# Kernel optimization log

Measured on AMD Instinct MI355X. Metric: run time of the kernel, lower is better.

The kernel has to match this reference:

```python
import jax, jax.numpy as jnp
import numpy as np

N_AGENTS = 32
STATE_DIM = 512
EMBED = 64
BATCH = 32768


def setup_inputs() -> dict:
    key = jax.random.key(0)
    ks = jax.random.split(key, 16)
    g = lambda k, shape, fan_in: jax.random.normal(k, shape, jnp.float32) / np.sqrt(fan_in)
    return {
        "agent_qs": jax.random.normal(ks[0], (BATCH, N_AGENTS), jnp.float32),
        "states": jax.random.normal(ks[1], (BATCH, STATE_DIM), jnp.float32),
        # hyper_w1: Linear(state,E) -> ReLU -> Linear(E, n_agents*E)
        "w1_l1_w": g(ks[2], (EMBED, STATE_DIM), STATE_DIM),
        "w1_l1_b": jnp.zeros((EMBED,), jnp.float32),
        "w1_l2_w": g(ks[3], (N_AGENTS * EMBED, EMBED), EMBED),
        "w1_l2_b": jnp.zeros((N_AGENTS * EMBED,), jnp.float32),
        # hyper_w2: Linear(state,E) -> ReLU -> Linear(E, E)
        "w2_l1_w": g(ks[4], (EMBED, STATE_DIM), STATE_DIM),
        "w2_l1_b": jnp.zeros((EMBED,), jnp.float32),
        "w2_l2_w": g(ks[5], (EMBED, EMBED), EMBED),
        "w2_l2_b": jnp.zeros((EMBED,), jnp.float32),
        # hyper_b1: Linear(state, E)
        "b1_w": g(ks[6], (EMBED, STATE_DIM), STATE_DIM),
        "b1_b": jnp.zeros((EMBED,), jnp.float32),
        # hyper_b2: Linear(state,E) -> ReLU -> Linear(E, 1)
        "b2_l1_w": g(ks[7], (EMBED, STATE_DIM), STATE_DIM),
        "b2_l1_b": jnp.zeros((EMBED,), jnp.float32),
        "b2_l2_w": g(ks[8], (1, EMBED), EMBED),
        "b2_l2_b": jnp.zeros((1,), jnp.float32),
    }


def _linear(x, w, b):
    return x @ w.T + b


def reference(agent_qs, states,
              w1_l1_w, w1_l1_b, w1_l2_w, w1_l2_b,
              w2_l1_w, w2_l1_b, w2_l2_w, w2_l2_b,
              b1_w, b1_b, b2_l1_w, b2_l1_b, b2_l2_w, b2_l2_b):
    B = agent_qs.shape[0]
    # hypernetworks producing per-sample weights
    w1 = jnp.abs(_linear(jax.nn.relu(_linear(states, w1_l1_w, w1_l1_b)), w1_l2_w, w1_l2_b))
    w1 = w1.reshape(B, N_AGENTS, EMBED)                      # [B, A, E]
    b1 = _linear(states, b1_w, b1_b)                         # [B, E]
    hidden = jax.nn.elu(jnp.einsum('ba,bae->be', agent_qs, w1) + b1)  # [B, E]
    w2 = jnp.abs(_linear(jax.nn.relu(_linear(states, w2_l1_w, w2_l1_b)), w2_l2_w, w2_l2_b))  # [B, E]
    b2 = _linear(jax.nn.relu(_linear(states, b2_l1_w, b2_l1_b)), b2_l2_w, b2_l2_b)           # [B, 1]
    q_total = jnp.einsum('be,be->b', hidden, w2) + b2[:, 0]  # [B]
    return q_total
```

## Files before the change

### kernel.cpp

```cpp
#include <hip/hip_runtime.h>

typedef unsigned short u16;
typedef unsigned int u32;
typedef short bf16x8 __attribute__((ext_vector_type(8)));
typedef float f32x4 __attribute__((ext_vector_type(4)));
typedef u16 u16x4 __attribute__((ext_vector_type(4)));

#define NAG 32
#define STATE 512
#define EMBED 64
#define TB 64

#define OFF_W1L1 0
#define OFF_W2L1 32768
#define OFF_B1W  65536
#define OFF_B2L1 98304
#define OFF_W1L2 131072
#define OFF_W2L2 262144
#define WS_TOTAL 266240

#define Y_STR    200
#define SB_OFF   12800
#define SB_STR   72
#define SB_BUF   (64 * 72)
#define W1BS_OFF 22016
#define QST_OFF  24064
#define QST_STR  68
#define PBUF_OFF 12800
#define PBUF_STR 72
#define PBUF_WV  (64 * 72)
#define QACC_OFF  31232
#define QACC2_OFF 31360
#define B2WV_OFF  31616
#define SMEM_U16  31744

__device__ __forceinline__ float bf2f(u16 u) {
    u32 i = ((u32)u) << 16; float f;
    __builtin_memcpy(&f, &i, 4); return f;
}
__device__ __forceinline__ u16 f2bf(float f) {
    u32 i; __builtin_memcpy(&i, &f, 4);
    return (u16)((i + 0x8000u) >> 16);
}
__device__ __forceinline__ bf16x8 ld8(const u16* p) {
    return *reinterpret_cast<const bf16x8*>(p);
}
__device__ __forceinline__ bf16x8 cvt8(f32x4 a, f32x4 b) {
    bf16x8 r;
#pragma unroll
    for (int i = 0; i < 4; ++i) r[i]     = (short)f2bf(a[i]);
#pragma unroll
    for (int i = 0; i < 4; ++i) r[i + 4] = (short)f2bf(b[i]);
    return r;
}

__global__ __launch_bounds__(256) void cvt_weights(
    const float* __restrict__ w1l1w, const float* __restrict__ w2l1w,
    const float* __restrict__ b1w,   const float* __restrict__ b2l1w,
    const float* __restrict__ w1l2w, const float* __restrict__ w2l2w,
    u16* __restrict__ ws)
{
    int idx = blockIdx.x * 256 + threadIdx.x;
    const float* src; int off;
    if      (idx < OFF_W2L1)  { src = w1l1w; off = OFF_W1L1; }
    else if (idx < OFF_B1W)   { src = w2l1w; off = OFF_W2L1; }
    else if (idx < OFF_B2L1)  { src = b1w;   off = OFF_B1W;  }
    else if (idx < OFF_W1L2)  { src = b2l1w; off = OFF_B2L1; }
    else if (idx < OFF_W2L2)  { src = w1l2w; off = OFF_W1L2; }
    else if (idx < WS_TOTAL)  { src = w2l2w; off = OFF_W2L2; }
    else return;
    ws[idx] = f2bf(src[idx - off]);
}

__global__ __launch_bounds__(512, 4) void qmix_kernel(
    const float* __restrict__ qs,    const float* __restrict__ st,
    const u16*  __restrict__ wsb,
    const float* __restrict__ w1l1b, const float* __restrict__ w1l2b,
    const float* __restrict__ w2l1b, const float* __restrict__ w2l2b,
    const float* __restrict__ b1b,   const float* __restrict__ b2l1b,
    const float* __restrict__ b2l2w, const float* __restrict__ b2l2b,
    float* __restrict__ out)
{
    __shared__ u16 smem[SMEM_U16];
    float* qaccF  = (float*)(smem + QACC_OFF);
    float* qacc2F = (float*)(smem + QACC2_OFF);
    float* b2wvF  = (float*)(smem + B2WV_OFF);

    const int t    = threadIdx.x;
    const int wave = t >> 6, lane = t & 63;
    const int m = lane & 15, quad = lane >> 4;
    const int sbase = blockIdx.x * TB;

    if (t < 64) b2wvF[t] = b2l2w[t];
    if (t < 256) {
        const float* qp = qs + (size_t)sbase * NAG + t * 8;
        f32x4 q0 = *reinterpret_cast<const f32x4*>(qp);
        f32x4 q1 = *reinterpret_cast<const f32x4*>(qp + 4);
        const int s = t >> 2, a0 = (t & 3) * 8;
#pragma unroll
        for (int j = 0; j < 4; ++j) smem[QST_OFF + (a0 + j) * QST_STR + s]     = f2bf(q0[j]);
#pragma unroll
        for (int j = 0; j < 4; ++j) smem[QST_OFF + (a0 + 4 + j) * QST_STR + s] = f2bf(q1[j]);
    } else {
        const int i = t & 255;
        f32x4 w0 = *reinterpret_cast<const f32x4*>(w1l2b + i * 8);
        f32x4 w1 = *reinterpret_cast<const f32x4*>(w1l2b + i * 8 + 4);
        *reinterpret_cast<bf16x8*>(&smem[W1BS_OFF + i * 8]) = cvt8(w0, w1);
    }

    const int ss1 = t >> 3, c8 = t & 7;
    const float* stb = st + (size_t)sbase * STATE;
    {
        const float* g1 = stb + (size_t)ss1 * STATE + c8 * 8;
        f32x4 a0 = *reinterpret_cast<const f32x4*>(g1);
        f32x4 a1 = *reinterpret_cast<const f32x4*>(g1 + 4);
        *reinterpret_cast<bf16x8*>(&smem[SB_OFF + ss1 * SB_STR + c8 * 8]) = cvt8(a0, a1);
    }

    const u16* wAw = wsb + (size_t)(wave * 32) * STATE;
    bf16x8 bfr[2][2][2];
#pragma unroll
    for (int ot = 0; ot < 2; ++ot) {
        const u16* wr = wAw + (size_t)(ot * 16 + m) * STATE + quad * 8;
        bfr[0][ot][0] = ld8(wr);
        bfr[0][ot][1] = ld8(wr + 32);
    }
    __syncthreads();

    f32x4 acc[4][2] = {};
#pragma unroll
    for (int ks = 0; ks < 8; ++ks) {
        f32x4 sa0 = {}, sa1 = {};
        if (ks < 7) {
            const float* g1 = stb + (size_t)ss1 * STATE + (ks + 1) * 64 + c8 * 8;
            sa0 = *reinterpret_cast<const f32x4*>(g1);
            sa1 = *reinterpret_cast<const f32x4*>(g1 + 4);
#pragma unroll
            for (int ot = 0; ot < 2; ++ot) {
                const u16* wr = wAw + (size_t)(ot * 16 + m) * STATE + (ks + 1) * 64 + quad * 8;
                bfr[(ks + 1) & 1][ot][0] = ld8(wr);
                bfr[(ks + 1) & 1][ot][1] = ld8(wr + 32);
            }
        }
        const u16* sbc = smem + SB_OFF + (ks & 1) * SB_BUF;
#pragma unroll
        for (int st2 = 0; st2 < 4; ++st2) {
            const int row = st2 * 16 + m;
            bf16x8 af0 = ld8(&sbc[row * SB_STR + quad * 8]);
            bf16x8 af1 = ld8(&sbc[row * SB_STR + (quad + 4) * 8]);
#pragma unroll
            for (int ot = 0; ot < 2; ++ot)
                acc[st2][ot] = __builtin_amdgcn_mfma_f32_16x16x32_bf16(af0, bfr[ks & 1][ot][0], acc[st2][ot], 0, 0, 0);
#pragma unroll
            for (int ot = 0; ot < 2; ++ot)
                acc[st2][ot] = __builtin_amdgcn_mfma_f32_16x16x32_bf16(af1, bfr[ks & 1][ot][1], acc[st2][ot], 0, 0, 0);
        }
        if (ks < 7) {
            u16* dst = smem + SB_OFF + ((ks + 1) & 1) * SB_BUF;
            *reinterpret_cast<bf16x8*>(&dst[ss1 * SB_STR + c8 * 8]) = cvt8(sa0, sa1);
        }
        __syncthreads();
    }

    {
        const int grp = wave >> 1, half = wave & 1;
        if (grp < 3) {
            const float* barr = (grp == 0) ? w1l1b : (grp == 1) ? w2l1b : b1b;
            const bool isrelu = (grp != 2);
            float wb[2];
#pragma unroll
            for (int ot = 0; ot < 2; ++ot) wb[ot] = barr[half * 32 + ot * 16 + m];
#pragma unroll
            for (int st2 = 0; st2 < 4; ++st2)
#pragma unroll
                for (int ot = 0; ot < 2; ++ot)
#pragma unroll
                    for (int r = 0; r < 4; ++r) {
                        float v = acc[st2][ot][r] + wb[ot];
                        if (isrelu) v = fmaxf(v, 0.f);
                        smem[(st2 * 16 + quad * 4 + r) * Y_STR + grp * 64 + half * 32 + ot * 16 + m] = f2bf(v);
                    }
        } else {
            float wb[2], bw[2];
#pragma unroll
            for (int ot = 0; ot < 2; ++ot) wb[ot] = b2l1b[half * 32 + ot * 16 + m];
#pragma unroll
            for (int ot = 0; ot < 2; ++ot) bw[ot] = b2wvF[half * 32 + ot * 16 + m];
#pragma unroll
            for (int st2 = 0; st2 < 4; ++st2)
#pragma unroll
                for (int r = 0; r < 4; ++r) {
                    float pd = 0.f;
#pragma unroll
                    for (int ot = 0; ot < 2; ++ot)
                        pd += fmaxf(acc[st2][ot][r] + wb[ot], 0.f) * bw[ot];
#pragma unroll
                    for (int off = 1; off < 16; off <<= 1) pd += __shfl_xor(pd, off, 64);
                    if (m == 0) qacc2F[half * 64 + st2 * 16 + quad * 4 + r] = pd;
                }
        }
    }
    __syncthreads();

    const int ah = wave & 3, sh = wave >> 2;
    bf16x8 h1f[2][2];
#pragma unroll
    for (int st2 = 0; st2 < 2; ++st2) {
        const int row = sh * 32 + st2 * 16 + m;
        h1f[st2][0] = ld8(&smem[row * Y_STR + quad * 8]);
        h1f[st2][1] = ld8(&smem[row * Y_STR + 32 + quad * 8]);
    }

    const u16* wB = wsb + OFF_W1L2 + (size_t)(ah * 8) * 64 * EMBED;
    f32x4 hacc[2][4] = {};
#pragma unroll
    for (int ag = 0; ag < 8; ++ag) {
        const int a = ah * 8 + ag;
        bf16x8 bb[4][2];
#pragma unroll
        for (int ot = 0; ot < 4; ++ot) {
            const u16* wr = wB + (size_t)(ag * 64 + ot * 16 + m) * EMBED + quad * 8;
            bb[ot][0] = ld8(wr);
            bb[ot][1] = ld8(wr + 32);
        }
        float bias[4];
#pragma unroll
        for (int ot = 0; ot < 4; ++ot) bias[ot] = bf2f(smem[W1BS_OFF + a * EMBED + ot * 16 + m]);
#pragma unroll
        for (int st2 = 0; st2 < 2; ++st2) {
            u16x4 qv = *reinterpret_cast<const u16x4*>(
                &smem[QST_OFF + a * QST_STR + sh * 32 + st2 * 16 + quad * 4]);
#pragma unroll
            for (int ot = 0; ot < 4; ++ot) {
                f32x4 p = {};
                p = __builtin_amdgcn_mfma_f32_16x16x32_bf16(h1f[st2][0], bb[ot][0], p, 0, 0, 0);
                p = __builtin_amdgcn_mfma_f32_16x16x32_bf16(h1f[st2][1], bb[ot][1], p, 0, 0, 0);
#pragma unroll
                for (int r = 0; r < 4; ++r)
                    hacc[st2][ot][r] += bf2f((u16)qv[r]) * fabsf(p[r] + bias[ot]);
            }
        }
    }
    __syncthreads();

#pragma unroll
    for (int st2 = 0; st2 < 2; ++st2)
#pragma unroll
        for (int ot = 0; ot < 4; ++ot)
#pragma unroll
            for (int r = 0; r < 4; ++r)
                smem[PBUF_OFF + ah * PBUF_WV
                     + (sh * 32 + st2 * 16 + quad * 4 + r) * PBUF_STR + ot * 16 + m]
                    = f2bf(hacc[st2][ot][r]);
    __syncthreads();

    {
        const int s  = t >> 3;
        const int eb = (t & 7) * 8;
        float v[8];
#pragma unroll
        for (int j = 0; j < 8; ++j) v[j] = 0.f;
#pragma unroll
        for (int pw = 0; pw < 4; ++pw) {
            u16x4 x0 = *reinterpret_cast<const u16x4*>(
                &smem[PBUF_OFF + pw * PBUF_WV + s * PBUF_STR + eb]);
            u16x4 x1 = *reinterpret_cast<const u16x4*>(
                &smem[PBUF_OFF + pw * PBUF_WV + s * PBUF_STR + eb + 4]);
#pragma unroll
            for (int j = 0; j < 4; ++j) v[j]     += bf2f((u16)x0[j]);
#pragma unroll
            for (int j = 0; j < 4; ++j) v[4 + j] += bf2f((u16)x1[j]);
        }
        bf16x8 bv = ld8(&smem[s * Y_STR + 128 + eb]);
        bf16x8 o;
#pragma unroll
        for (int j = 0; j < 8; ++j) {
            float h = v[j] + bf2f((u16)bv[j]);
            h = (h > 0.f) ? h : (__expf(h) - 1.f);
            o[j] = (short)f2bf(h);
        }
        *reinterpret_cast<bf16x8*>(&smem[s * Y_STR + 128 + eb]) = o;
    }
    __syncthreads();

    if (wave < 4) {
        const int s0 = wave * 16;
        bf16x8 h2f0 = ld8(&smem[(s0 + m) * Y_STR + 64 + quad * 8]);
        bf16x8 h2f1 = ld8(&smem[(s0 + m) * Y_STR + 96 + quad * 8]);

        f32x4 qp = {};
#pragma unroll
        for (int tp = 0; tp < 4; ++tp) {
            const u16* wc = wsb + OFF_W2L2 + (size_t)(tp * 16 + m) * EMBED + quad * 8;
            bf16x8 c0 = ld8(wc);
            bf16x8 c1 = ld8(wc + 32);
            f32x4 p = {};
            p = __builtin_amdgcn_mfma_f32_16x16x32_bf16(h2f0, c0, p, 0, 0, 0);
            p = __builtin_amdgcn_mfma_f32_16x16x32_bf16(h2f1, c1, p, 0, 0, 0);
            const float bias = w2l2b[tp * 16 + m];
#pragma unroll
            for (int r = 0; r < 4; ++r)
                qp[r] += bf2f(smem[(s0 + quad * 4 + r) * Y_STR + 128 + tp * 16 + m]) * fabsf(p[r] + bias);
        }
#pragma unroll
        for (int off = 1; off < 16; off <<= 1) {
#pragma unroll
            for (int r = 0; r < 4; ++r) qp[r] += __shfl_xor(qp[r], off, 64);
        }
        if (m == 0) {
#pragma unroll
            for (int r = 0; r < 4; ++r) qaccF[s0 + quad * 4 + r] = qp[r];
        }
    }
    __syncthreads();

    if (t < TB) out[sbase + t] = qaccF[t] + qacc2F[t] + qacc2F[64 + t] + b2l2b[0];
}

extern "C" void kernel_launch(void* const* d_in, const int* in_sizes, int n_in,
                              void* d_out, int out_size, void* d_ws, size_t ws_size,
                              hipStream_t stream)
{
    const float* qs    = (const float*)d_in[0];
    const float* st    = (const float*)d_in[1];
    const float* w1l1w = (const float*)d_in[2];
    const float* w1l1b = (const float*)d_in[3];
    const float* w1l2w = (const float*)d_in[4];
    const float* w1l2b = (const float*)d_in[5];
    const float* w2l1w = (const float*)d_in[6];
    const float* w2l1b = (const float*)d_in[7];
    const float* w2l2w = (const float*)d_in[8];
    const float* w2l2b = (const float*)d_in[9];
    const float* b1w   = (const float*)d_in[10];
    const float* b1b   = (const float*)d_in[11];
    const float* b2l1w = (const float*)d_in[12];
    const float* b2l1b = (const float*)d_in[13];
    const float* b2l2w = (const float*)d_in[14];
    const float* b2l2b = (const float*)d_in[15];

    u16* wsb = (u16*)d_ws;

    cvt_weights<<<(WS_TOTAL + 255) / 256, 256, 0, stream>>>(
        w1l1w, w2l1w, b1w, b2l1w, w1l2w, w2l2w, wsb);

    int B = in_sizes[0] / NAG;
    int grid = B / TB;
    qmix_kernel<<<grid, 512, 0, stream>>>(
        qs, st, wsb,
        w1l1b, w1l2b, w2l1b, w2l2b, b1b, b2l1b, b2l2w, b2l2b,
        (float*)d_out);
}
```

Measured before the change: 168.5 us.

## Halve per-block sample tile and use 256-thread blocks with wider per-wave outputs

Cuts the samples per block from 64 to 32 and the block size from 512 to 256 threads, so the grid doubles. Each wave now computes all 64 outputs of one hypernetwork first layer instead of half of one, and later stages are remapped to match. The register double-buffering of weight fragments is replaced by loading them at the start of each k-step, and the final barrier of the k-loop is dropped. In exchange, the bf16 weights are re-read from cache twice as often per sample, and weight-load latency is less hidden.

```diff
diff --git a/kernel.cpp b/kernel.cpp
--- a/kernel.cpp
+++ b/kernel.cpp
@@ -9,7 +9,7 @@
 #define NAG 32
 #define STATE 512
 #define EMBED 64
-#define TB 64
+#define TB 32
 
 #define OFF_W1L1 0
 #define OFF_W2L1 32768
@@ -19,20 +19,21 @@
 #define OFF_W2L2 262144
 #define WS_TOTAL 266240
 
+#define Y_OFF    0
 #define Y_STR    200
-#define SB_OFF   12800
+#define SB_OFF   6400
 #define SB_STR   72
-#define SB_BUF   (64 * 72)
-#define W1BS_OFF 22016
-#define QST_OFF  24064
-#define QST_STR  68
-#define PBUF_OFF 12800
+#define SB_BUF   (32 * 72)
+#define W1BS_OFF 11008
+#define QST_OFF  13056
+#define QST_STR  36
+#define PBUF_OFF 6400
 #define PBUF_STR 72
-#define PBUF_WV  (64 * 72)
-#define QACC_OFF  31232
-#define QACC2_OFF 31360
-#define B2WV_OFF  31616
-#define SMEM_U16  31744
+#define PBUF_WV  (32 * 72)
+#define QACC_OFF  15616
+#define QACC2_OFF 15680
+#define B2WV_OFF  15744
+#define SMEM_U16  15872
 
 __device__ __forceinline__ float bf2f(u16 u) {
     u32 i = ((u32)u) << 16; float f;
@@ -72,7 +73,7 @@
     ws[idx] = f2bf(src[idx - off]);
 }
 
-__global__ __launch_bounds__(512, 4) void qmix_kernel(
+__global__ __launch_bounds__(256, 4) void qmix_kernel(
     const float* __restrict__ qs,    const float* __restrict__ st,
     const u16*  __restrict__ wsb,
     const float* __restrict__ w1l1b, const float* __restrict__ w1l2b,
@@ -92,7 +93,7 @@
     const int sbase = blockIdx.x * TB;
 
     if (t < 64) b2wvF[t] = b2l2w[t];
-    if (t < 256) {
+    if (t < 128) {
         const float* qp = qs + (size_t)sbase * NAG + t * 8;
         f32x4 q0 = *reinterpret_cast<const f32x4*>(qp);
         f32x4 q1 = *reinterpret_cast<const f32x4*>(qp + 4);
@@ -101,11 +102,11 @@
         for (int j = 0; j < 4; ++j) smem[QST_OFF + (a0 + j) * QST_STR + s]     = f2bf(q0[j]);
 #pragma unroll
         for (int j = 0; j < 4; ++j) smem[QST_OFF + (a0 + 4 + j) * QST_STR + s] = f2bf(q1[j]);
-    } else {
-        const int i = t & 255;
-        f32x4 w0 = *reinterpret_cast<const f32x4*>(w1l2b + i * 8);
-        f32x4 w1 = *reinterpret_cast<const f32x4*>(w1l2b + i * 8 + 4);
-        *reinterpret_cast<bf16x8*>(&smem[W1BS_OFF + i * 8]) = cvt8(w0, w1);
+    }
+    {
+        f32x4 w0 = *reinterpret_cast<const f32x4*>(w1l2b + t * 8);
+        f32x4 w1 = *reinterpret_cast<const f32x4*>(w1l2b + t * 8 + 4);
+        *reinterpret_cast<bf16x8*>(&smem[W1BS_OFF + t * 8]) = cvt8(w0, w1);
     }
 
     const int ss1 = t >> 3, c8 = t & 7;
@@ -117,105 +118,95 @@
         *reinterpret_cast<bf16x8*>(&smem[SB_OFF + ss1 * SB_STR + c8 * 8]) = cvt8(a0, a1);
     }
 
-    const u16* wAw = wsb + (size_t)(wave * 32) * STATE;
-    bf16x8 bfr[2][2][2];
-#pragma unroll
-    for (int ot = 0; ot < 2; ++ot) {
-        const u16* wr = wAw + (size_t)(ot * 16 + m) * STATE + quad * 8;
-        bfr[0][ot][0] = ld8(wr);
-        bfr[0][ot][1] = ld8(wr + 32);
-    }
-    __syncthreads();
-
-    f32x4 acc[4][2] = {};
+    const u16* wAw = wsb + (size_t)(wave * 64) * STATE;
+    __syncthreads();
+
+    f32x4 acc[2][4] = {};
 #pragma unroll
     for (int ks = 0; ks < 8; ++ks) {
+        bf16x8 bfr[4][2];
+#pragma unroll
+        for (int ot = 0; ot < 4; ++ot) {
+            const u16* wr = wAw + (size_t)(ot * 16 + m) * STATE + ks * 64 + quad * 8;
+            bfr[ot][0] = ld8(wr);
+            bfr[ot][1] = ld8(wr + 32);
+        }
         f32x4 sa0 = {}, sa1 = {};
         if (ks < 7) {
             const float* g1 = stb + (size_t)ss1 * STATE + (ks + 1) * 64 + c8 * 8;
             sa0 = *reinterpret_cast<const f32x4*>(g1);
             sa1 = *reinterpret_cast<const f32x4*>(g1 + 4);
-#pragma unroll
-            for (int ot = 0; ot < 2; ++ot) {
-                const u16* wr = wAw + (size_t)(ot * 16 + m) * STATE + (ks + 1) * 64 + quad * 8;
-                bfr[(ks + 1) & 1][ot][0] = ld8(wr);
-                bfr[(ks + 1) & 1][ot][1] = ld8(wr + 32);
-            }
         }
         const u16* sbc = smem + SB_OFF + (ks & 1) * SB_BUF;
 #pragma unroll
-        for (int st2 = 0; st2 < 4; ++st2) {
+        for (int st2 = 0; st2 < 2; ++st2) {
             const int row = st2 * 16 + m;
             bf16x8 af0 = ld8(&sbc[row * SB_STR + quad * 8]);
             bf16x8 af1 = ld8(&sbc[row * SB_STR + (quad + 4) * 8]);
 #pragma unroll
-            for (int ot = 0; ot < 2; ++ot)
-                acc[st2][ot] = __builtin_amdgcn_mfma_f32_16x16x32_bf16(af0, bfr[ks & 1][ot][0], acc[st2][ot], 0, 0, 0);
-#pragma unroll
-            for (int ot = 0; ot < 2; ++ot)
-                acc[st2][ot] = __builtin_amdgcn_mfma_f32_16x16x32_bf16(af1, bfr[ks & 1][ot][1], acc[st2][ot], 0, 0, 0);
+            for (int ot = 0; ot < 4; ++ot)
+                acc[st2][ot] = __builtin_amdgcn_mfma_f32_16x16x32_bf16(af0, bfr[ot][0], acc[st2][ot], 0, 0, 0);
+#pragma unroll
+            for (int ot = 0; ot < 4; ++ot)
+                acc[st2][ot] = __builtin_amdgcn_mfma_f32_16x16x32_bf16(af1, bfr[ot][1], acc[st2][ot], 0, 0, 0);
         }
         if (ks < 7) {
             u16* dst = smem + SB_OFF + ((ks + 1) & 1) * SB_BUF;
             *reinterpret_cast<bf16x8*>(&dst[ss1 * SB_STR + c8 * 8]) = cvt8(sa0, sa1);
-        }
-        __syncthreads();
-    }
-
-    {
-        const int grp = wave >> 1, half = wave & 1;
-        if (grp < 3) {
-            const float* barr = (grp == 0) ? w1l1b : (grp == 1) ? w2l1b : b1b;
-            const bool isrelu = (grp != 2);
-            float wb[2];
-#pragma unroll
-            for (int ot = 0; ot < 2; ++ot) wb[ot] = barr[half * 32 + ot * 16 + m];
-#pragma unroll
-            for (int st2 = 0; st2 < 4; ++st2)
-#pragma unroll
-                for (int ot = 0; ot < 2; ++ot)
-#pragma unroll
-                    for (int r = 0; r < 4; ++r) {
-                        float v = acc[st2][ot][r] + wb[ot];
-                        if (isrelu) v = fmaxf(v, 0.f);
-                        smem[(st2 * 16 + quad * 4 + r) * Y_STR + grp * 64 + half * 32 + ot * 16 + m] = f2bf(v);
-                    }
-        } else {
-            float wb[2], bw[2];
-#pragma unroll
-            for (int ot = 0; ot < 2; ++ot) wb[ot] = b2l1b[half * 32 + ot * 16 + m];
-#pragma unroll
-            for (int ot = 0; ot < 2; ++ot) bw[ot] = b2wvF[half * 32 + ot * 16 + m];
-#pragma unroll
-            for (int st2 = 0; st2 < 4; ++st2)
+            __syncthreads();
+        }
+    }
+
+    if (wave < 3) {
+        const float* barr = (wave == 0) ? w1l1b : (wave == 1) ? w2l1b : b1b;
+        const bool isrelu = (wave != 2);
+        float wb[4];
+#pragma unroll
+        for (int ot = 0; ot < 4; ++ot) wb[ot] = barr[ot * 16 + m];
+#pragma unroll
+        for (int st2 = 0; st2 < 2; ++st2)
+#pragma unroll
+            for (int ot = 0; ot < 4; ++ot)
 #pragma unroll
                 for (int r = 0; r < 4; ++r) {
-                    float pd = 0.f;
-#pragma unroll
-                    for (int ot = 0; ot < 2; ++ot)
-                        pd += fmaxf(acc[st2][ot][r] + wb[ot], 0.f) * bw[ot];
-#pragma unroll
-                    for (int off = 1; off < 16; off <<= 1) pd += __shfl_xor(pd, off, 64);
-                    if (m == 0) qacc2F[half * 64 + st2 * 16 + quad * 4 + r] = pd;
+                    float v = acc[st2][ot][r] + wb[ot];
+                    if (isrelu) v = fmaxf(v, 0.f);
+                    smem[Y_OFF + (st2 * 16 + quad * 4 + r) * Y_STR + wave * 64 + ot * 16 + m] = f2bf(v);
                 }
-        }
-    }
-    __syncthreads();
-
-    const int ah = wave & 3, sh = wave >> 2;
+    } else {
+        float wb[4], bw[4];
+#pragma unroll
+        for (int ot = 0; ot < 4; ++ot) wb[ot] = b2l1b[ot * 16 + m];
+#pragma unroll
+        for (int ot = 0; ot < 4; ++ot) bw[ot] = b2wvF[ot * 16 + m];
+#pragma unroll
+        for (int st2 = 0; st2 < 2; ++st2)
+#pragma unroll
+            for (int r = 0; r < 4; ++r) {
+                float pd = 0.f;
+#pragma unroll
+                for (int ot = 0; ot < 4; ++ot)
+                    pd += fmaxf(acc[st2][ot][r] + wb[ot], 0.f) * bw[ot];
+#pragma unroll
+                for (int off = 1; off < 16; off <<= 1) pd += __shfl_xor(pd, off, 64);
+                if (m == 0) qacc2F[st2 * 16 + quad * 4 + r] = pd;
+            }
+    }
+    __syncthreads();
+
     bf16x8 h1f[2][2];
 #pragma unroll
     for (int st2 = 0; st2 < 2; ++st2) {
-        const int row = sh * 32 + st2 * 16 + m;
-        h1f[st2][0] = ld8(&smem[row * Y_STR + quad * 8]);
-        h1f[st2][1] = ld8(&smem[row * Y_STR + 32 + quad * 8]);
-    }
-
-    const u16* wB = wsb + OFF_W1L2 + (size_t)(ah * 8) * 64 * EMBED;
+        const int row = st2 * 16 + m;
+        h1f[st2][0] = ld8(&smem[Y_OFF + row * Y_STR + quad * 8]);
+        h1f[st2][1] = ld8(&smem[Y_OFF + row * Y_STR + 32 + quad * 8]);
+    }
+
+    const u16* wB = wsb + OFF_W1L2 + (size_t)(wave * 8) * 64 * EMBED;
     f32x4 hacc[2][4] = {};
 #pragma unroll
     for (int ag = 0; ag < 8; ++ag) {
-        const int a = ah * 8 + ag;
+        const int a = wave * 8 + ag;
         bf16x8 bb[4][2];
 #pragma unroll
         for (int ot = 0; ot < 4; ++ot) {
@@ -229,7 +220,7 @@
 #pragma unroll
         for (int st2 = 0; st2 < 2; ++st2) {
             u16x4 qv = *reinterpret_cast<const u16x4*>(
-                &smem[QST_OFF + a * QST_STR + sh * 32 + st2 * 16 + quad * 4]);
+                &smem[QST_OFF + a * QST_STR + st2 * 16 + quad * 4]);
 #pragma unroll
             for (int ot = 0; ot < 4; ++ot) {
                 f32x4 p = {};
@@ -249,8 +240,8 @@
         for (int ot = 0; ot < 4; ++ot)
 #pragma unroll
             for (int r = 0; r < 4; ++r)
-                smem[PBUF_OFF + ah * PBUF_WV
-                     + (sh * 32 + st2 * 16 + quad * 4 + r) * PBUF_STR + ot * 16 + m]
+                smem[PBUF_OFF + wave * PBUF_WV
+                     + (st2 * 16 + quad * 4 + r) * PBUF_STR + ot * 16 + m]
                     = f2bf(hacc[st2][ot][r]);
     __syncthreads();
 
@@ -271,7 +262,7 @@
 #pragma unroll
             for (int j = 0; j < 4; ++j) v[4 + j] += bf2f((u16)x1[j]);
         }
-        bf16x8 bv = ld8(&smem[s * Y_STR + 128 + eb]);
+        bf16x8 bv = ld8(&smem[Y_OFF + s * Y_STR + 128 + eb]);
         bf16x8 o;
 #pragma unroll
         for (int j = 0; j < 8; ++j) {
@@ -279,14 +270,14 @@
             h = (h > 0.f) ? h : (__expf(h) - 1.f);
             o[j] = (short)f2bf(h);
         }
-        *reinterpret_cast<bf16x8*>(&smem[s * Y_STR + 128 + eb]) = o;
-    }
-    __syncthreads();
-
-    if (wave < 4) {
+        *reinterpret_cast<bf16x8*>(&smem[Y_OFF + s * Y_STR + 128 + eb]) = o;
+    }
+    __syncthreads();
+
+    if (wave < 2) {
         const int s0 = wave * 16;
-        bf16x8 h2f0 = ld8(&smem[(s0 + m) * Y_STR + 64 + quad * 8]);
-        bf16x8 h2f1 = ld8(&smem[(s0 + m) * Y_STR + 96 + quad * 8]);
+        bf16x8 h2f0 = ld8(&smem[Y_OFF + (s0 + m) * Y_STR + 64 + quad * 8]);
+        bf16x8 h2f1 = ld8(&smem[Y_OFF + (s0 + m) * Y_STR + 96 + quad * 8]);
 
         f32x4 qp = {};
 #pragma unroll
@@ -300,7 +291,8 @@
             const float bias = w2l2b[tp * 16 + m];
 #pragma unroll
             for (int r = 0; r < 4; ++r)
-                qp[r] += bf2f(smem[(s0 + quad * 4 + r) * Y_STR + 128 + tp * 16 + m]) * fabsf(p[r] + bias);
+                qp[r] += bf2f(smem[Y_OFF + (s0 + quad * 4 + r) * Y_STR + 128 + tp * 16 + m])
+                         * fabsf(p[r] + bias);
         }
 #pragma unroll
         for (int off = 1; off < 16; off <<= 1) {
@@ -314,7 +306,7 @@
     }
     __syncthreads();
 
-    if (t < TB) out[sbase + t] = qaccF[t] + qacc2F[t] + qacc2F[64 + t] + b2l2b[0];
+    if (t < TB) out[sbase + t] = qaccF[t] + qacc2F[t] + b2l2b[0];
 }
 
 extern "C" void kernel_launch(void* const* d_in, const int* in_sizes, int n_in,
@@ -345,7 +337,7 @@
 
     int B = in_sizes[0] / NAG;
     int grid = B / TB;
-    qmix_kernel<<<grid, 512, 0, stream>>>(
+    qmix_kernel<<<grid, 256, 0, stream>>>(
         qs, st, wsb,
         w1l1b, w1l2b, w2l1b, w2l2b, b1b, b2l1b, b2l2w, b2l2b,
         (float*)d_out);
```

Result: slower. 184.9 us (+9.7%).
